# Performance work log

Hardware: AMD Instinct MI355X
Metric: run time of the kernel (lower is better)

## Reference

```python
import jax, jax.numpy as jnp
import numpy as np

SCALES = [2 ** i for i in range(11)]  # init: scales=10 -> [1,2,...,1024]
B, N, C, K = 8, 1024, 256, 4096


def setup_inputs() -> dict:
    key = jax.random.key(0)
    k1, k2, k3 = jax.random.split(key, 3)
    f_BNC = jax.random.normal(k1, (B, N, C), dtype=jnp.float32)
    base = jax.random.normal(k2, (K, C), dtype=jnp.float32)          # orthogonal-init codebook base
    proj_w = jax.random.normal(k3, (C, C), dtype=jnp.float32) / np.float32(np.sqrt(C))  # xavier-ish
    proj_b = jnp.zeros((C,), dtype=jnp.float32)
    return {"f_BNC": f_BNC, "base": base, "proj_w": proj_w, "proj_b": proj_b}


def _linear_interp(x, out_size):
    # x: [B, C, n] -> [B, C, out_size], matches F.interpolate(mode='linear', align_corners=False)
    n = x.shape[-1]
    scale = n / out_size
    src = jnp.maximum((jnp.arange(out_size, dtype=jnp.float32) + 0.5) * scale - 0.5, 0.0)
    i0 = jnp.floor(src).astype(jnp.int32)
    i1 = jnp.minimum(i0 + 1, n - 1)
    w = (src - i0.astype(jnp.float32)).astype(x.dtype)
    return x[..., i0] * (1.0 - w) + x[..., i1] * w


def reference(f_BNC, base, proj_w, proj_b):
    sg = jax.lax.stop_gradient
    # update_embedding(): embedding = proj(base)
    embedding = base @ proj_w.T + proj_b                 # [K, C]
    emb_ng = sg(embedding)
    e_sq = jnp.sum(emb_ng * emb_ng, axis=1)              # [K]

    f_BCN = jnp.transpose(f_BNC, (0, 2, 1))              # [B, C, N]
    f_ng = sg(f_BCN)
    f_rest = f_ng
    f_hat = jnp.zeros_like(f_ng)
    commit = jnp.float32(0.0)
    qlat = jnp.float32(0.0)
    SN = len(SCALES)

    for pn in SCALES:
        # area interpolation == exact mean pooling since N % pn == 0
        rest_BCp = f_rest.reshape(B, C, pn, N // pn).mean(axis=-1)       # [B, C, pn]
        q = jnp.transpose(rest_BCp, (0, 2, 1)).reshape(-1, C)            # [B*pn, C]
        # squared-distance to codebook (gradients never flow through d: argmin only)
        d = jnp.sum(q * q, axis=1, keepdims=True) + e_sq - 2.0 * (q @ emb_ng.T)  # [B*pn, K]
        idx = jnp.argmin(d, axis=1)                                      # [B*pn]
        h_BnC = embedding[idx].reshape(B, pn, C)                         # gather (grad flows to codebook)
        h_BCn = _linear_interp(jnp.transpose(h_BnC, (0, 2, 1)), N)       # [B, C, N]
        f_hat = f_hat + h_BCn
        # residual feeds only argmin at the next scale -> dead gradient path in torch too
        f_rest = f_rest - sg(h_BCn)
        commit = commit + 0.25 * jnp.mean((sg(f_hat) - f_BCN) ** 2)
        qlat = qlat + jnp.mean((f_hat - f_ng) ** 2)

    commit = commit / SN
    qlat = qlat / SN
    # straight-through: f_hat = (f_hat.data - f_no_grad) + f_BCN
    f_out = sg(f_hat) - f_ng + f_BCN
    return (jnp.transpose(f_out, (0, 2, 1)), commit, qlat)
```

## Files before the change

kernel.cpp:

```cpp
#include <hip/hip_runtime.h>
#include <cfloat>

#define BB 8
#define NN 1024
#define CC 256
#define KK 4096
#define SN 11
#define BNC (BB*NN*CC)
#define RMAX 8192

typedef __attribute__((ext_vector_type(8))) _Float16 half8;
typedef __attribute__((ext_vector_type(4))) float f32x4;

__device__ __forceinline__ void split2(float v, ushort& h, ushort& l) {
    union { _Float16 f; ushort u; } a, b;
    a.f = (_Float16)v;
    b.f = (_Float16)(v - (float)a.f);
    h = a.u; l = b.u;
}

__global__ __launch_bounds__(256) void embed_prep(
    const float* __restrict__ base, const float* __restrict__ pw,
    const float* __restrict__ pb, const float* __restrict__ f,
    float* __restrict__ emb, ushort* __restrict__ eh, ushort* __restrict__ el,
    float* __restrict__ esq, float* __restrict__ p16) {
    int blk = blockIdx.x;
    int t = threadIdx.x;
    if (blk >= 256) {
        int bb = blk - 256;
        int c4 = t & 63;
        const float4* src = (const float4*)(f + (size_t)bb * 16 * CC) + c4;
        float4 s = make_float4(0.f, 0.f, 0.f, 0.f);
#pragma unroll
        for (int j = 0; j < 16; ++j) {
            float4 v = src[(size_t)j * 64];
            s.x += v.x; s.y += v.y; s.z += v.z; s.w += v.w;
        }
        ((float4*)(p16 + (size_t)bb * CC))[c4] = s;
        return;
    }
    __shared__ float bs[16][CC];
    __shared__ float wpart[16][4];
    int k0 = blk * 16;
    int w = t >> 6, lane = t & 63;
    for (int i = t; i < 16 * CC; i += 256) bs[i >> 8][i & 255] = base[k0 * CC + i];
    __syncthreads();
    float acc[16];
#pragma unroll
    for (int m = 0; m < 16; ++m) acc[m] = 0.f;
    for (int j = 0; j < CC; ++j) {
        float wv = pw[t * CC + j];
#pragma unroll
        for (int m = 0; m < 16; ++m) acc[m] += bs[m][j] * wv;
    }
    float bias = pb[t];
#pragma unroll
    for (int m = 0; m < 16; ++m) {
        float v = acc[m] + bias;
        int o = (k0 + m) * CC + t;
        emb[o] = v;
        ushort h, l;
        split2(64.f * v, h, l);
        eh[o] = h; el[o] = l;
        float sq = v * v;
#pragma unroll
        for (int d = 1; d < 64; d <<= 1) sq += __shfl_xor(sq, d);
        if (lane == 0) wpart[m][w] = sq;
    }
    __syncthreads();
    if (t < 16) esq[k0 + t] = wpart[t][0] + wpart[t][1] + wpart[t][2] + wpart[t][3];
}

__global__ __launch_bounds__(256, 4) void dist_small(
    const float* __restrict__ src, const float* __restrict__ emb,
    const float* __restrict__ esq, int R, int g16, int pn, float inv,
    float* __restrict__ pval, int* __restrict__ pidx) {
    __shared__ float qs[32][CC];
    __shared__ float es[64][33];
    int t = threadIdx.x;
    int ws = t >> 6, j = t & 63;
    int k0 = blockIdx.x * 64;
    int r0c = blockIdx.y * 32;
    {
        int row = t >> 3;
        int f4b = (t & 7) * 8;
        int gr = r0c + row;
        float4 a4[8];
#pragma unroll
        for (int ii = 0; ii < 8; ++ii) a4[ii] = make_float4(0.f, 0.f, 0.f, 0.f);
        if (gr < R) {
            int b = gr / pn, p = gr - b * pn;
            const float4* sp = (const float4*)(src + ((size_t)b * 64 + (size_t)p * g16) * CC) + f4b;
            for (int i = 0; i < g16; ++i) {
#pragma unroll
                for (int ii = 0; ii < 8; ++ii) {
                    float4 v = sp[ii];
                    a4[ii].x += v.x; a4[ii].y += v.y; a4[ii].z += v.z; a4[ii].w += v.w;
                }
                sp += 64;
            }
        }
#pragma unroll
        for (int ii = 0; ii < 8; ++ii) {
            a4[ii].x *= inv; a4[ii].y *= inv; a4[ii].z *= inv; a4[ii].w *= inv;
            *(float4*)&qs[row][(f4b + ii) * 4] = a4[ii];
        }
    }
    float acc[8];
#pragma unroll
    for (int ri = 0; ri < 8; ++ri) acc[ri] = 0.f;
    for (int ck = 0; ck < 8; ++ck) {
        __syncthreads();
        {
            int code = t >> 2, cb = (t & 3) * 8;
            float4 v0 = *(const float4*)&emb[(size_t)(k0 + code) * CC + ck * 32 + cb];
            float4 v1 = *(const float4*)&emb[(size_t)(k0 + code) * CC + ck * 32 + cb + 4];
            es[code][cb + 0] = v0.x; es[code][cb + 1] = v0.y;
            es[code][cb + 2] = v0.z; es[code][cb + 3] = v0.w;
            es[code][cb + 4] = v1.x; es[code][cb + 5] = v1.y;
            es[code][cb + 6] = v1.z; es[code][cb + 7] = v1.w;
        }
        __syncthreads();
        for (int c = 0; c < 32; ++c) {
            float ev = es[j][c];
#pragma unroll
            for (int ri = 0; ri < 8; ++ri)
                acc[ri] += qs[ws + 4 * ri][ck * 32 + c] * ev;
        }
    }
    float esv = esq[k0 + j];
#pragma unroll
    for (int ri = 0; ri < 8; ++ri) {
        int r = r0c + ws + 4 * ri;
        if (r >= R) continue;
        float v = esv - 2.f * acc[ri];
        int bi = k0 + j;
#pragma unroll
        for (int d = 1; d < 64; d <<= 1) {
            float ov = __shfl_xor(v, d);
            int oi = __shfl_xor(bi, d);
            if (ov < v || (ov == v && oi < bi)) { v = ov; bi = oi; }
        }
        if (j == 0) {
            pval[(size_t)r * 64 + blockIdx.x] = v;
            pidx[(size_t)r * 64 + blockIdx.x] = bi;
        }
    }
}

__global__ __launch_bounds__(256, 2) void dist_mfma(
    const ushort* __restrict__ qh, const ushort* __restrict__ ql,
    const ushort* __restrict__ eh, const ushort* __restrict__ el,
    const float* __restrict__ esq,
    float* __restrict__ pval, int* __restrict__ pidx) {
    __shared__ ushort tiles[4096 * 8];
    __shared__ float wv[2][128];
    __shared__ int wi[2][128];
    int t = threadIdx.x;
    int w = t >> 6, lane = t & 63;
    int l15 = lane & 15, hi = lane >> 4;
    int wr = w >> 1, wc = w & 1;
    int r0 = blockIdx.x * 128;
    int kb = blockIdx.y;
    int k0 = kb * 128;

    f32x4 acc[4][4];
#pragma unroll
    for (int mi = 0; mi < 4; ++mi)
#pragma unroll
        for (int ni = 0; ni < 4; ++ni) acc[mi][ni] = (f32x4){0.f, 0.f, 0.f, 0.f};

    for (int ck = 0; ck < 4; ++ck) {
        __syncthreads();
#pragma unroll
        for (int it = 0; it < 16; ++it) {
            int s = it * 256 + t;
            const ushort* g;
            if (s < 2048) {
                int a = s >> 10;
                int rem = s & 1023;
                int row = rem >> 3, sr = rem & 7;
                int c = (ck << 6) + ((sr ^ (row & 7)) << 3);
                g = (a ? ql : qh) + (size_t)(r0 + row) * CC + c;
            } else {
                int s2 = s - 2048;
                int b = s2 >> 10;
                int rem = s2 & 1023;
                int kcol = rem >> 3, sr = rem & 7;
                int c = (ck << 6) + ((sr ^ (kcol & 7)) << 3);
                g = (b ? el : eh) + (size_t)(k0 + kcol) * CC + c;
            }
            ushort* lb = &tiles[(size_t)(it * 256 + (w << 6)) * 8];
            __builtin_amdgcn_global_load_lds(
                (const __attribute__((address_space(1))) unsigned int*)g,
                (__attribute__((address_space(3))) unsigned int*)lb, 16, 0, 0);
        }
        __syncthreads();

#pragma unroll
        for (int kk = 0; kk < 2; ++kk) {
            int cs = (kk << 2) + hi;
            half8 bf0[4], bf1[4], af[4];
#pragma unroll
            for (int ni = 0; ni < 4; ++ni) {
                int kcol = (wc << 6) + (ni << 4) + l15;
                int sb = 2048 + (kcol << 3) + (cs ^ (kcol & 7));
                bf0[ni] = *(const half8*)&tiles[sb * 8];
                bf1[ni] = *(const half8*)&tiles[(sb + 1024) * 8];
            }
#pragma unroll
            for (int mi = 0; mi < 4; ++mi) {
                int row = (wr << 6) + (mi << 4) + l15;
                af[mi] = *(const half8*)&tiles[((row << 3) + (cs ^ (row & 7))) * 8];
            }
#pragma unroll
            for (int mi = 0; mi < 4; ++mi)
#pragma unroll
                for (int ni = 0; ni < 4; ++ni)
                    acc[mi][ni] = __builtin_amdgcn_mfma_f32_16x16x32_f16(af[mi], bf0[ni], acc[mi][ni], 0, 0, 0);
#pragma unroll
            for (int mi = 0; mi < 4; ++mi)
#pragma unroll
                for (int ni = 0; ni < 4; ++ni)
                    acc[mi][ni] = __builtin_amdgcn_mfma_f32_16x16x32_f16(af[mi], bf1[ni], acc[mi][ni], 0, 0, 0);
#pragma unroll
            for (int mi = 0; mi < 4; ++mi) {
                int row = (wr << 6) + (mi << 4) + l15;
                af[mi] = *(const half8*)&tiles[(1024 + (row << 3) + (cs ^ (row & 7))) * 8];
            }
#pragma unroll
            for (int mi = 0; mi < 4; ++mi)
#pragma unroll
                for (int ni = 0; ni < 4; ++ni)
                    acc[mi][ni] = __builtin_amdgcn_mfma_f32_16x16x32_f16(af[mi], bf0[ni], acc[mi][ni], 0, 0, 0);
        }
    }

    int cbase = k0 + (wc << 6) + l15;
    float es4[4];
#pragma unroll
    for (int ni = 0; ni < 4; ++ni) es4[ni] = 4096.f * esq[cbase + ni * 16];
#pragma unroll
    for (int mi = 0; mi < 4; ++mi) {
#pragma unroll
        for (int reg = 0; reg < 4; ++reg) {
            float v = es4[0] - 2.f * acc[mi][0][reg];
            int i = cbase;
#pragma unroll
            for (int ni = 1; ni < 4; ++ni) {
                float v1 = es4[ni] - 2.f * acc[mi][ni][reg];
                if (v1 < v) { v = v1; i = cbase + ni * 16; }
            }
#pragma unroll
            for (int d = 1; d < 16; d <<= 1) {
                float ov = __shfl_xor(v, d);
                int oi = __shfl_xor(i, d);
                if (ov < v || (ov == v && oi < i)) { v = ov; i = oi; }
            }
            if (l15 == 0) {
                int row = (wr << 6) + (mi << 4) + (hi << 2) + reg;
                wv[wc][row] = v;
                wi[wc][row] = i;
            }
        }
    }
    __syncthreads();
    if (t < 128) {
        float v = wv[0][t];
        int i = wi[0][t];
        float ov = wv[1][t];
        int oi = wi[1][t];
        if (ov < v || (ov == v && oi < i)) { v = ov; i = oi; }
        pval[(size_t)(r0 + t) * 64 + kb] = v;
        pidx[(size_t)(r0 + t) * 64 + kb] = i;
    }
}

__global__ __launch_bounds__(256) void update_pool(
    const float* __restrict__ emb, const float* __restrict__ pval,
    const int* __restrict__ pidx, const float* __restrict__ rin,
    float* __restrict__ rout, const float* __restrict__ f,
    float* __restrict__ outp, float* __restrict__ parts,
    ushort* __restrict__ qh, ushort* __restrict__ ql,
    float* __restrict__ qf, float* __restrict__ p16u,
    int pn, int gn, int pnn, int ks, int finalflag) {
    int blk = blockIdx.x;
    int b = blk >> 6, n16 = blk & 63;
    int t = threadIdx.x;
    int w = t >> 6, lane = t & 63;
    int n0 = n16 * 16;
    const float scale = (float)pn * (1.0f / 1024.0f);
    float s_lo = (n0 + 0.5f) * scale - 0.5f;
    if (s_lo < 0.f) s_lo = 0.f;
    int r_lo = (int)s_lo;
    float s_hi = (n0 + 15.5f) * scale - 0.5f;
    if (s_hi < 0.f) s_hi = 0.f;
    int r_hi = min((int)s_hi + 1, pn - 1);
    int cnt = r_hi - r_lo + 1;
    __shared__ int sidx[20];
    for (int ri = w; ri < cnt; ri += 4) {
        size_t rowg = (size_t)(b * pn + r_lo + ri) * 64;
        float v = (lane < ks) ? pval[rowg + lane] : FLT_MAX;
        int i = (lane < ks) ? pidx[rowg + lane] : 0x7fffffff;
#pragma unroll
        for (int d = 1; d < 64; d <<= 1) {
            float ov = __shfl_xor(v, d);
            int oi = __shfl_xor(i, d);
            if (ov < v || (ov == v && oi < i)) { v = ov; i = oi; }
        }
        if (lane == 0) sidx[ri] = i;
    }
    __syncthreads();
    __shared__ float4 rlds[16][64];
    __shared__ float wred[4];
    int nsub = t >> 6;
    int c4 = t & 63;
    float sq = 0.f;
#pragma unroll
    for (int jj = 0; jj < 4; ++jj) {
        int j = nsub + 4 * jj;
        int n = n0 + j;
        float s = (n + 0.5f) * scale - 0.5f;
        if (s < 0.f) s = 0.f;
        int i0 = (int)s;
        float wgt = s - (float)i0;
        int i1 = min(i0 + 1, pn - 1);
        int k0 = sidx[i0 - r_lo];
        int k1 = sidx[i1 - r_lo];
        float4 e0 = ((const float4*)(emb + (size_t)k0 * CC))[c4];
        float4 e1 = ((const float4*)(emb + (size_t)k1 * CC))[c4];
        float wm = 1.f - wgt;
        float4 h = make_float4(wm * e0.x + wgt * e1.x, wm * e0.y + wgt * e1.y,
                               wm * e0.z + wgt * e1.z, wm * e0.w + wgt * e1.w);
        size_t o4 = ((size_t)b * NN + n) * 64 + c4;
        float4 rv0 = ((const float4*)rin)[o4];
        float4 rv = make_float4(rv0.x - h.x, rv0.y - h.y, rv0.z - h.z, rv0.w - h.w);
        if (!finalflag) {
            ((float4*)rout)[o4] = rv;
        } else {
            float4 fv = ((const float4*)f)[o4];
            ((float4*)outp)[o4] = make_float4(fv.x - rv.x, fv.y - rv.y,
                                              fv.z - rv.z, fv.w - rv.w);
        }
        sq += rv.x * rv.x + rv.y * rv.y + rv.z * rv.z + rv.w * rv.w;
        rlds[j][c4] = rv;
    }
    for (int off = 32; off > 0; off >>= 1) sq += __shfl_down(sq, off);
    if (lane == 0) wred[w] = sq;
    __syncthreads();
    if (t == 0) parts[blk] = wred[0] + wred[1] + wred[2] + wred[3];
    if (gn == 0) return;
    const float* rl = (const float*)rlds;
    if (gn < 16) {
        float pr = 0.f;
        for (int j = 0; j < 16; ++j) {
            pr += rl[j * CC + t];
            if ((j & (gn - 1)) == (gn - 1)) {
                float mean = pr * (1.f / (float)gn);
                ushort H, L;
                split2(64.f * mean, H, L);
                size_t r = (size_t)b * pnn + (size_t)((n0 + j) / gn);
                qh[r * CC + t] = H;
                ql[r * CC + t] = L;
                pr = 0.f;
            }
        }
    } else {
        float pr = 0.f;
        for (int j = 0; j < 16; ++j) pr += rl[j * CC + t];
        if (gn == 16) qf[(size_t)blk * CC + t] = pr * (1.f / 16.f);
        else p16u[(size_t)blk * CC + t] = pr;
    }
}

__global__ void reduce_final(const float* __restrict__ parts, float* __restrict__ out) {
    __shared__ float red[256];
    int t = threadIdx.x;
    float s = 0.f;
    for (int i = t; i < SN * 512; i += 256) s += parts[i];
    red[t] = s;
    __syncthreads();
    for (int k = 128; k > 0; k >>= 1) {
        if (t < k) red[t] += red[t + k];
        __syncthreads();
    }
    if (t == 0) {
        float mean_sum = red[0] / (float)BNC;
        out[BNC] = 0.25f * mean_sum / (float)SN;
        out[BNC + 1] = mean_sum / (float)SN;
    }
}

extern "C" void kernel_launch(void* const* d_in, const int* in_sizes, int n_in,
                              void* d_out, int out_size, void* d_ws, size_t ws_size,
                              hipStream_t stream) {
    const float* f    = (const float*)d_in[0];
    const float* base = (const float*)d_in[1];
    const float* pw   = (const float*)d_in[2];
    const float* pb   = (const float*)d_in[3];
    float* out = (float*)d_out;

    float* emb   = (float*)d_ws;
    float* esq   = emb + (size_t)KK * CC;
    float* pwT   = esq + KK;
    float* parts = pwT + (size_t)CC * CC;
    float* pval  = parts + (size_t)SN * 512;
    float* p16   = pval + (size_t)RMAX * 64;
    float* p16u  = p16 + (size_t)BB * 64 * CC;
    float* qf    = p16u + (size_t)BB * 64 * CC;
    float* resid = qf + (size_t)512 * CC;
    int*   pidx  = (int*)(resid + BNC);
    ushort* eh = (ushort*)(pidx + (size_t)RMAX * 64);
    ushort* el = eh + (size_t)KK * CC;
    ushort* qh = el + (size_t)KK * CC;
    ushort* ql = qh + (size_t)RMAX * CC;

    embed_prep<<<768, 256, 0, stream>>>(base, pw, pb, f, emb, eh, el, esq, p16);

    for (int sidx = 0; sidx < SN; ++sidx) {
        int pn = 1 << sidx;
        int R = BB * pn;
        int ks;
        if (pn <= 64) {
            const float* src;
            float inv;
            int g16;
            if (pn == 64)      { src = qf;   g16 = 1;       inv = 1.f; }
            else if (pn == 1)  { src = p16;  g16 = 64;      inv = 1.f / 1024.f; }
            else               { src = p16u; g16 = 64 / pn; inv = 1.f / (16.f * (64 / pn)); }
            dim3 grid(64, (R + 31) / 32);
            dist_small<<<grid, 256, 0, stream>>>(src, emb, esq, R, g16, pn, inv, pval, pidx);
            ks = 64;
        } else {
            dist_mfma<<<dim3(R / 128, 32), 256, 0, stream>>>(qh, ql, eh, el, esq, pval, pidx);
            ks = 32;
        }
        int pnn = (sidx < SN - 1) ? (pn << 1) : 0;
        int gn = pnn ? (NN / pnn) : 0;
        const float* rin = (sidx == 0) ? f : resid;
        update_pool<<<BB * 64, 256, 0, stream>>>(emb, pval, pidx, rin, resid, f, out,
                                                 parts + (size_t)sidx * 512,
                                                 qh, ql, qf, p16u, pn, gn, pnn, ks,
                                                 (sidx == SN - 1) ? 1 : 0);
    }
    reduce_final<<<1, 256, 0, stream>>>(parts, out);
}
```

Before: 550.6 us.

## Compute coarse-scale queries algebraically and fuse first seven residual updates

For scales 1..64 the full-resolution residual update pass is no longer run. A small combineQ kernel builds the next-scale pooled query directly from precomputed 16-row pooled sums of f, minus the interpolated codebook contributions of earlier scales. A single bigpass kernel then applies all seven coarse-scale updates to f in one sweep, producing the residual, the per-scale loss partial sums and the fp16-split queries for scale 128. This removes six full read/write passes over the 8 MB residual, at the cost of redundant per-block argmin reductions and serial interpolation-weight loops in combineQ.

```diff
diff --git a/kernel.cpp b/kernel.cpp
--- a/kernel.cpp
+++ b/kernel.cpp
@@ -73,7 +73,7 @@
 
 __global__ __launch_bounds__(256, 4) void dist_small(
     const float* __restrict__ src, const float* __restrict__ emb,
-    const float* __restrict__ esq, int R, int g16, int pn, float inv,
+    const float* __restrict__ esq, int R, int g16, int pn, int srow, float inv,
     float* __restrict__ pval, int* __restrict__ pidx) {
     __shared__ float qs[32][CC];
     __shared__ float es[64][33];
@@ -90,7 +90,7 @@
         for (int ii = 0; ii < 8; ++ii) a4[ii] = make_float4(0.f, 0.f, 0.f, 0.f);
         if (gr < R) {
             int b = gr / pn, p = gr - b * pn;
-            const float4* sp = (const float4*)(src + ((size_t)b * 64 + (size_t)p * g16) * CC) + f4b;
+            const float4* sp = (const float4*)(src + ((size_t)b * srow + (size_t)p * g16) * CC) + f4b;
             for (int i = 0; i < g16; ++i) {
 #pragma unroll
                 for (int ii = 0; ii < 8; ++ii) {
@@ -144,6 +144,162 @@
         if (j == 0) {
             pval[(size_t)r * 64 + blockIdx.x] = v;
             pidx[(size_t)r * 64 + blockIdx.x] = bi;
+        }
+    }
+}
+
+__global__ __launch_bounds__(256) void combineQ(
+    const float* __restrict__ pvS, const int* __restrict__ piS,
+    const float* __restrict__ p16, const float* __restrict__ emb,
+    float* __restrict__ qf, int sc, int pn_next) {
+    int r = blockIdx.x;
+    int b = r / pn_next, p = r - b * pn_next;
+    int g = 1024 / pn_next;
+    int g16 = 64 / pn_next;
+    int t = threadIdx.x, w = t >> 6, lane = t & 63;
+    __shared__ int sidx[64];
+    int nitems = (2 << sc) - 1;
+    for (int item = w; item < nitems; item += 4) {
+        int jj = 31 - __builtin_clz(item + 1);
+        int q = item + 1 - (1 << jj);
+        size_t rowg = ((size_t)BB * ((1u << jj) - 1) + (size_t)b * (1 << jj) + q) * 64;
+        float v = pvS[rowg + lane];
+        int ii = piS[rowg + lane];
+#pragma unroll
+        for (int d = 1; d < 64; d <<= 1) {
+            float ov = __shfl_xor(v, d);
+            int oi = __shfl_xor(ii, d);
+            if (ov < v || (ov == v && oi < ii)) { v = ov; ii = oi; }
+        }
+        if (lane == 0) sidx[item] = ii;
+    }
+    __syncthreads();
+    float base = 0.f;
+    for (int i = 0; i < g16; ++i)
+        base += p16[((size_t)b * 64 + (size_t)p * g16 + i) * CC + t];
+    float hsum = 0.f;
+    for (int j = 0; j <= sc; ++j) {
+        int pnj = 1 << j, off = pnj - 1;
+        int curi0 = -1, curi1 = 0;
+        float c0 = 0.f, c1 = 0.f;
+        for (int n = p * g; n < p * g + g; ++n) {
+            float s = (n + 0.5f) * (float)pnj * (1.f / 1024.f) - 0.5f;
+            if (s < 0.f) s = 0.f;
+            int i0 = (int)s;
+            float wq = s - (float)i0;
+            if (i0 != curi0) {
+                if (curi0 >= 0)
+                    hsum += c0 * emb[(size_t)sidx[off + curi0] * CC + t]
+                          + c1 * emb[(size_t)sidx[off + curi1] * CC + t];
+                curi0 = i0;
+                curi1 = min(i0 + 1, pnj - 1);
+                c0 = 0.f; c1 = 0.f;
+            }
+            c0 += 1.f - wq;
+            c1 += wq;
+        }
+        hsum += c0 * emb[(size_t)sidx[off + curi0] * CC + t]
+              + c1 * emb[(size_t)sidx[off + curi1] * CC + t];
+    }
+    qf[(size_t)r * CC + t] = base * (1.f / (16.f * (float)g16)) - hsum * (1.f / (float)g);
+}
+
+__global__ __launch_bounds__(256) void bigpass(
+    const float* __restrict__ f, const float* __restrict__ emb,
+    const float* __restrict__ pvS, const int* __restrict__ piS,
+    float* __restrict__ resid, float* __restrict__ parts,
+    ushort* __restrict__ qh, ushort* __restrict__ ql) {
+    int blk = blockIdx.x;
+    int b = blk >> 6, n16 = blk & 63;
+    int t = threadIdx.x;
+    int w = t >> 6, lane = t & 63;
+    int n0 = n16 * 16;
+    __shared__ int sidx7[7][4];
+    __shared__ float4 rlds[16][64];
+    __shared__ float wred7[7][4];
+    int combo = 0;
+    for (int j = 0; j < 7; ++j) {
+        int pnj = 1 << j;
+        int rowoff = BB * (pnj - 1);
+        float sl = (n0 + 0.5f) * (float)pnj * (1.f / 1024.f) - 0.5f;
+        if (sl < 0.f) sl = 0.f;
+        int rlo = (int)sl;
+        float sh = (n0 + 15.5f) * (float)pnj * (1.f / 1024.f) - 0.5f;
+        if (sh < 0.f) sh = 0.f;
+        int rhi = min((int)sh + 1, pnj - 1);
+        for (int ri = 0; ri <= rhi - rlo; ++ri, ++combo) {
+            if ((combo & 3) == w) {
+                size_t rowg = (size_t)(rowoff + b * pnj + rlo + ri) * 64;
+                float v = pvS[rowg + lane];
+                int ii = piS[rowg + lane];
+#pragma unroll
+                for (int d = 1; d < 64; d <<= 1) {
+                    float ov = __shfl_xor(v, d);
+                    int oi = __shfl_xor(ii, d);
+                    if (ov < v || (ov == v && oi < ii)) { v = ov; ii = oi; }
+                }
+                if (lane == 0) sidx7[j][ri] = ii;
+            }
+        }
+    }
+    __syncthreads();
+    int nsub = t >> 6;
+    int c4 = t & 63;
+    float sq[7];
+#pragma unroll
+    for (int j = 0; j < 7; ++j) sq[j] = 0.f;
+#pragma unroll
+    for (int jj = 0; jj < 4; ++jj) {
+        int j16 = nsub + 4 * jj;
+        int n = n0 + j16;
+        size_t o4 = ((size_t)b * NN + n) * 64 + c4;
+        float4 r = ((const float4*)f)[o4];
+#pragma unroll
+        for (int j = 0; j < 7; ++j) {
+            int pnj = 1 << j;
+            float s = (n + 0.5f) * (float)pnj * (1.f / 1024.f) - 0.5f;
+            if (s < 0.f) s = 0.f;
+            int i0 = (int)s;
+            float wgt = s - (float)i0;
+            int i1 = min(i0 + 1, pnj - 1);
+            float sl = (n0 + 0.5f) * (float)pnj * (1.f / 1024.f) - 0.5f;
+            if (sl < 0.f) sl = 0.f;
+            int rlo = (int)sl;
+            int k0 = sidx7[j][i0 - rlo];
+            int k1 = sidx7[j][i1 - rlo];
+            float4 e0 = ((const float4*)(emb + (size_t)k0 * CC))[c4];
+            float4 e1 = ((const float4*)(emb + (size_t)k1 * CC))[c4];
+            float wm = 1.f - wgt;
+            r.x -= wm * e0.x + wgt * e1.x;
+            r.y -= wm * e0.y + wgt * e1.y;
+            r.z -= wm * e0.z + wgt * e1.z;
+            r.w -= wm * e0.w + wgt * e1.w;
+            sq[j] += r.x * r.x + r.y * r.y + r.z * r.z + r.w * r.w;
+        }
+        ((float4*)resid)[o4] = r;
+        rlds[j16][c4] = r;
+    }
+#pragma unroll
+    for (int j = 0; j < 7; ++j) {
+        float s = sq[j];
+        for (int off = 32; off > 0; off >>= 1) s += __shfl_down(s, off);
+        if (lane == 0) wred7[j][w] = s;
+    }
+    __syncthreads();
+    if (t < 7) parts[(size_t)t * 512 + blk] =
+        wred7[t][0] + wred7[t][1] + wred7[t][2] + wred7[t][3];
+    const float* rl = (const float*)rlds;
+    float pr = 0.f;
+    for (int j16 = 0; j16 < 16; ++j16) {
+        pr += rl[j16 * CC + t];
+        if ((j16 & 7) == 7) {
+            float mean = pr * 0.125f;
+            ushort H, L;
+            split2(64.f * mean, H, L);
+            size_t r = (size_t)b * 128 + (size_t)((n0 + j16) >> 3);
+            qh[r * CC + t] = H;
+            ql[r * CC + t] = L;
+            pr = 0.f;
         }
     }
 }
@@ -282,7 +438,6 @@
     float* __restrict__ rout, const float* __restrict__ f,
     float* __restrict__ outp, float* __restrict__ parts,
     ushort* __restrict__ qh, ushort* __restrict__ ql,
-    float* __restrict__ qf, float* __restrict__ p16u,
     int pn, int gn, int pnn, int ks, int finalflag) {
     int blk = blockIdx.x;
     int b = blk >> 6, n16 = blk & 63;
@@ -351,7 +506,7 @@
     if (t == 0) parts[blk] = wred[0] + wred[1] + wred[2] + wred[3];
     if (gn == 0) return;
     const float* rl = (const float*)rlds;
-    if (gn < 16) {
+    {
         float pr = 0.f;
         for (int j = 0; j < 16; ++j) {
             pr += rl[j * CC + t];
@@ -365,11 +520,6 @@
                 pr = 0.f;
             }
         }
-    } else {
-        float pr = 0.f;
-        for (int j = 0; j < 16; ++j) pr += rl[j * CC + t];
-        if (gn == 16) qf[(size_t)blk * CC + t] = pr * (1.f / 16.f);
-        else p16u[(size_t)blk * CC + t] = pr;
     }
 }
 
@@ -402,8 +552,8 @@
 
     float* emb   = (float*)d_ws;
     float* esq   = emb + (size_t)KK * CC;
-    float* pwT   = esq + KK;
-    float* parts = pwT + (size_t)CC * CC;
+    float* pad0  = esq + KK;
+    float* parts = pad0 + (size_t)CC * CC;
     float* pval  = parts + (size_t)SN * 512;
     float* p16   = pval + (size_t)RMAX * 64;
     float* p16u  = p16 + (size_t)BB * 64 * CC;
@@ -414,33 +564,39 @@
     ushort* el = eh + (size_t)KK * CC;
     ushort* qh = el + (size_t)KK * CC;
     ushort* ql = qh + (size_t)RMAX * CC;
+    float* pvalS = p16u;
+    int*   pidxS = (int*)(p16u + 65536);
 
     embed_prep<<<768, 256, 0, stream>>>(base, pw, pb, f, emb, eh, el, esq, p16);
 
-    for (int sidx = 0; sidx < SN; ++sidx) {
+    for (int sidx = 0; sidx <= 6; ++sidx) {
         int pn = 1 << sidx;
         int R = BB * pn;
-        int ks;
-        if (pn <= 64) {
-            const float* src;
-            float inv;
-            int g16;
-            if (pn == 64)      { src = qf;   g16 = 1;       inv = 1.f; }
-            else if (pn == 1)  { src = p16;  g16 = 64;      inv = 1.f / 1024.f; }
-            else               { src = p16u; g16 = 64 / pn; inv = 1.f / (16.f * (64 / pn)); }
-            dim3 grid(64, (R + 31) / 32);
-            dist_small<<<grid, 256, 0, stream>>>(src, emb, esq, R, g16, pn, inv, pval, pidx);
-            ks = 64;
+        size_t rowoff = (size_t)BB * (pn - 1) * 64;
+        dim3 grid(64, (R + 31) / 32);
+        if (sidx == 0)
+            dist_small<<<grid, 256, 0, stream>>>(p16, emb, esq, R, 64, 1, 64,
+                                                 1.f / 1024.f, pvalS + rowoff, pidxS + rowoff);
+        else
+            dist_small<<<grid, 256, 0, stream>>>(qf, emb, esq, R, 1, pn, pn,
+                                                 1.f, pvalS + rowoff, pidxS + rowoff);
+        if (sidx < 6) {
+            int pnn = pn << 1;
+            combineQ<<<BB * pnn, 256, 0, stream>>>(pvalS, pidxS, p16, emb, qf, sidx, pnn);
         } else {
-            dist_mfma<<<dim3(R / 128, 32), 256, 0, stream>>>(qh, ql, eh, el, esq, pval, pidx);
-            ks = 32;
-        }
+            bigpass<<<512, 256, 0, stream>>>(f, emb, pvalS, pidxS, resid, parts, qh, ql);
+        }
+    }
+
+    for (int sidx = 7; sidx < SN; ++sidx) {
+        int pn = 1 << sidx;
+        int R = BB * pn;
+        dist_mfma<<<dim3(R / 128, 32), 256, 0, stream>>>(qh, ql, eh, el, esq, pval, pidx);
         int pnn = (sidx < SN - 1) ? (pn << 1) : 0;
         int gn = pnn ? (NN / pnn) : 0;
-        const float* rin = (sidx == 0) ? f : resid;
-        update_pool<<<BB * 64, 256, 0, stream>>>(emb, pval, pidx, rin, resid, f, out,
+        update_pool<<<BB * 64, 256, 0, stream>>>(emb, pval, pidx, resid, resid, f, out,
                                                  parts + (size_t)sidx * 512,
-                                                 qh, ql, qf, p16u, pn, gn, pnn, ks,
+                                                 qh, ql, pn, gn, pnn, 32,
                                                  (sidx == SN - 1) ? 1 : 0);
     }
     reduce_final<<<1, 256, 0, stream>>>(parts, out);
```

Measured after the change: 634.1 us. 1.15x slower.
